# Performance work log

Measured on AMD Instinct MI355X. Metric: run time of the kernel, lower is better.

The kernel has to match this reference:

```python
import jax, jax.numpy as jnp
import numpy as np

B, N, E = 2, 25000, 400000
FC_IN, FC_HID = 64, 256
MUL = 32                     # multiplicity of each output irrep (0e,1e,2e)
W_NUMEL = 3 * MUL            # 96 tensor-product weights per edge
NUM_NEIGHBORS = 16.0


def setup_inputs() -> dict:
    key = jax.random.key(0)
    k1, k2, k3, k4, k5, k6 = jax.random.split(key, 6)
    return {
        "edge_src": jax.random.randint(k1, (E,), 0, N),
        "edge_dst": jax.random.randint(k2, (E,), 0, N),
        "node_emb": jax.random.normal(k3, (B, N, 3), jnp.float32),
        "edge_type": jax.random.normal(k4, (E, FC_IN), jnp.float32),
        "W1": jax.random.normal(k5, (FC_IN, FC_HID), jnp.float32),
        "W2": jax.random.normal(k6, (FC_HID, W_NUMEL), jnp.float32),
    }


def _tensor_product(x, y, w):
    """1o x 1o -> 32x0e + 32x1e + 32x2e, per-edge uvw weights.
    x, y: (B,E,3); w: (E,96). Component-normalized CG coefficients."""
    inv3 = 1.0 / np.sqrt(3.0)
    inv2 = 1.0 / np.sqrt(2.0)
    inv6 = 1.0 / np.sqrt(6.0)
    w0, w1, w2 = w[:, :MUL], w[:, MUL:2 * MUL], w[:, 2 * MUL:]
    # l=0 path: dot product
    s = jnp.sum(x * y, axis=-1) * inv3                     # (B,E)
    out0 = w0[None] * s[..., None]                         # (B,E,32)
    # l=1 path: cross product
    v = jnp.cross(x, y) * inv2                             # (B,E,3)
    out1 = (w1[None, :, :, None] * v[:, :, None, :]).reshape(B, E, 3 * MUL)
    # l=2 path: symmetric traceless combinations
    x0, x1, x2 = x[..., 0], x[..., 1], x[..., 2]
    y0, y1, y2 = y[..., 0], y[..., 1], y[..., 2]
    t = jnp.stack([
        (x0 * y1 + x1 * y0) * inv2,
        (x1 * y2 + x2 * y1) * inv2,
        (x0 * y2 + x2 * y0) * inv2,
        (x0 * y0 - x1 * y1) * inv2,
        (2.0 * x2 * y2 - x0 * y0 - x1 * y1) * inv6,
    ], axis=-1)                                            # (B,E,5)
    out2 = (w2[None, :, :, None] * t[:, :, None, :]).reshape(B, E, 5 * MUL)
    return jnp.concatenate([out0, out1, out2], axis=-1)    # (B,E,288)


def reference(edge_src, edge_dst, node_emb, edge_type, W1, W2):
    # per-edge FC generating TP weights (e3nn FullyConnectedNet-style fan-in norm)
    h = jax.nn.silu(edge_type @ W1 * (1.0 / np.sqrt(FC_IN)))   # (E,256)
    w = (h @ W2) * (1.0 / np.sqrt(FC_HID))                     # (E,96)
    src_emb = node_emb[:, edge_src]                            # (B,E,3)
    dst_emb = node_emb[:, edge_dst]                            # (B,E,3)
    edge_message = _tensor_product(src_emb, dst_emb, w)        # (B,E,288)
    out = jnp.zeros((B, N, edge_message.shape[-1]), edge_message.dtype)
    out = out.at[:, edge_dst].add(edge_message)                # scatter-sum over dst
    return out * (1.0 / np.sqrt(NUM_NEIGHBORS))
```

## Files before the change

### kernel.cpp

```cpp
#include <hip/hip_runtime.h>

#define EDGES 400000
#define NN 25000
#define NCH 288
#define EPA 64
#define NBIN_PAD 25024
#define SWS 68

#define W1FRAG 16384
#define W2FRAG 24576

typedef float f32x4 __attribute__((ext_vector_type(4)));
typedef short short8 __attribute__((ext_vector_type(8)));

__device__ __forceinline__ unsigned short f2bf(float x) {
    unsigned u = __float_as_uint(x);
    unsigned r = (u + 0x7fffu + ((u >> 16) & 1u)) >> 16;
    return (unsigned short)r;
}
__device__ __forceinline__ unsigned short f2bf_t(float x) {
    return (unsigned short)(__float_as_uint(x) >> 16);
}
__device__ __forceinline__ float bf2f(unsigned short h) {
    return __uint_as_float(((unsigned)h) << 16);
}
__device__ __forceinline__ unsigned cvtpk(float a, float b) {
    unsigned r;
    asm("v_cvt_pk_bf16_f32 %0, %1, %2" : "=v"(r) : "v"(a), "v"(b));
    return r;
}
__device__ __forceinline__ float lowf(unsigned u)  { return __uint_as_float(u << 16); }
__device__ __forceinline__ float highf(unsigned u) { return __uint_as_float(u & 0xffff0000u); }

__global__ void k_wfrag(const float* __restrict__ W1, const float* __restrict__ W2,
                        unsigned short* __restrict__ w1h, unsigned short* __restrict__ w1l,
                        unsigned short* __restrict__ w2h, unsigned short* __restrict__ w2l) {
    int i = blockIdx.x * 256 + threadIdx.x;
    if (i < W1FRAG) {
        int j = i & 7, l = (i >> 3) & 63, nt = (i >> 9) & 15, k2 = (i >> 13) & 1;
        int n = nt * 16 + (l & 15), k = k2 * 32 + ((l >> 4) * 8) + j;
        float v = W1[k * 256 + n] * 0.125f;
        unsigned short hb = f2bf(v);
        w1h[i] = hb; w1l[i] = f2bf_t(v - bf2f(hb));
    } else if (i < W1FRAG + W2FRAG) {
        int i2 = i - W1FRAG;
        int j = i2 & 7, l = (i2 >> 3) & 63, r = i2 >> 9;
        int nt = r % 6, k8 = r / 6;
        int n = nt * 16 + (l & 15), k = k8 * 32 + ((l >> 4) * 8) + j;
        float v = W2[k * 96 + n] * 0.015625f;
        unsigned short hb = f2bf(v);
        w2h[i2] = hb; w2l[i2] = f2bf_t(v - bf2f(hb));
    }
}

__global__ void k_hist(const int* __restrict__ edst, unsigned* __restrict__ cnt) {
    int i = blockIdx.x * 256 + threadIdx.x;
    if (i < EDGES) atomicAdd(&cnt[edst[i]], 1u);
}

__global__ __launch_bounds__(1024) void k_scan(const unsigned* __restrict__ cnt,
                                               unsigned* __restrict__ cur) {
    __shared__ unsigned s_wt[16];
    __shared__ unsigned s_carry;
    const int t = threadIdx.x, lane = t & 63, wid = t >> 6;
    if (t == 0) s_carry = 0u;
    __syncthreads();
    for (int base = 0; base < NN; base += 1024) {
        int i = base + t;
        unsigned v = (i < NN) ? cnt[i] : 0u;
        unsigned incl = v;
        #pragma unroll
        for (int d = 1; d < 64; d <<= 1) {
            unsigned u = __shfl_up(incl, d);
            if (lane >= d) incl += u;
        }
        if (lane == 63) s_wt[wid] = incl;
        __syncthreads();
        if (wid == 0 && lane < 16) {
            unsigned wincl = s_wt[lane];
            #pragma unroll
            for (int d = 1; d < 16; d <<= 1) {
                unsigned u = __shfl_up(wincl, d);
                if (lane >= d) wincl += u;
            }
            s_wt[lane] = wincl;
        }
        __syncthreads();
        unsigned waveoff = (wid > 0) ? s_wt[wid - 1] : 0u;
        unsigned carry = s_carry;
        if (i < NN) cur[i] = carry + waveoff + incl - v;
        __syncthreads();
        if (t == 1023) s_carry = carry + s_wt[15];
        __syncthreads();
    }
}

__global__ void k_perm(const int* __restrict__ edst, unsigned* __restrict__ cur,
                       unsigned* __restrict__ perm) {
    int i = blockIdx.x * 256 + threadIdx.x;
    if (i < EDGES) {
        unsigned p = atomicAdd(&cur[edst[i]], 1u);
        perm[p] = (unsigned)i;
    }
}

struct SMemU {
    union {
        struct __align__(16) {
            unsigned short a1h[EPA * 64];
            unsigned short a1l[EPA * 64];
            unsigned short a2h[EPA * 64];
            unsigned short a2l[EPA * 64];
        };
        float sw[96 * SWS];
    };
};

template <bool SORTED>
__global__ __launch_bounds__(256) void conv_fused(
    const int* __restrict__ esrc, const int* __restrict__ edst,
    const float* __restrict__ nemb, const float* __restrict__ etype,
    const unsigned short* __restrict__ w1h, const unsigned short* __restrict__ w1l,
    const unsigned short* __restrict__ w2h, const unsigned short* __restrict__ w2l,
    const unsigned* __restrict__ perm,
    float* __restrict__ out)
{
    __shared__ SMemU U;
    __shared__ __align__(16) float gsm[2][9][SWS];
    __shared__ int s_eidx[EPA], s_dst[EPA];
    __shared__ unsigned s_mlo, s_mhi;

    const int t = threadIdx.x;
    const int lane = t & 63, w = t >> 6;
    const int g = lane >> 4, ln15 = lane & 15;
    const size_t slot0 = (size_t)blockIdx.x * EPA;

    if (t < EPA) {
        int e = SORTED ? (int)perm[slot0 + t] : (int)(slot0 + t);
        s_eidx[t] = e;
        s_dst[t] = edst[e];
    }
    __syncthreads();

    #pragma unroll
    for (int i = 0; i < 4; ++i) {
        int f4 = t + 256 * i;
        int row = f4 >> 4, q = f4 & 15;
        const float4* src = (const float4*)(etype + (size_t)s_eidx[row] * 64);
        float4 v = src[q];
        unsigned hp01 = cvtpk(v.x, v.y), hp23 = cvtpk(v.z, v.w);
        float lo0 = v.x - lowf(hp01), lo1 = v.y - highf(hp01);
        float lo2 = v.z - lowf(hp23), lo3 = v.w - highf(hp23);
        unsigned lp01 = cvtpk(lo0, lo1), lp23 = cvtpk(lo2, lo3);
        int boff = row * 128 + ((q * 8) ^ ((row & 7) << 4));
        *(uint2*)((char*)U.a1h + boff) = make_uint2(hp01, hp23);
        *(uint2*)((char*)U.a1l + boff) = make_uint2(lp01, lp23);
    }
    if (t < EPA * 2) {
        int e = t >> 1, b = t & 1;
        int sn = esrc[s_eidx[e]], dn = s_dst[e];
        const float* xp = nemb + ((size_t)b * NN + sn) * 3;
        const float* yp = nemb + ((size_t)b * NN + dn) * 3;
        float x0 = xp[0], x1 = xp[1], x2 = xp[2];
        float y0 = yp[0], y1 = yp[1], y2 = yp[2];
        const float inv3 = 0.5773502691896258f;
        const float inv2 = 0.7071067811865476f;
        const float inv6 = 0.4082482904638630f;
        gsm[b][0][e] = (x0*y0 + x1*y1 + x2*y2) * inv3;
        gsm[b][1][e] = (x1*y2 - x2*y1) * inv2;
        gsm[b][2][e] = (x2*y0 - x0*y2) * inv2;
        gsm[b][3][e] = (x0*y1 - x1*y0) * inv2;
        gsm[b][4][e] = (x0*y1 + x1*y0) * inv2;
        gsm[b][5][e] = (x1*y2 + x2*y1) * inv2;
        gsm[b][6][e] = (x0*y2 + x2*y0) * inv2;
        gsm[b][7][e] = (x0*y0 - x1*y1) * inv2;
        gsm[b][8][e] = (2.0f*x2*y2 - x0*y0 - x1*y1) * inv6;
    } else if (t < 192) {
        int e = t - 128;
        bool flag = (e > 0) && (s_dst[e] != s_dst[e - 1]);
        unsigned long long bal = __ballot(flag);
        if (e == 0) { s_mlo = (unsigned)bal; s_mhi = (unsigned)(bal >> 32); }
    }
    __syncthreads();

    const int mh = w & 1, nb = 3 * (w >> 1);
    f32x4 acc2[2][3];
    #pragma unroll
    for (int mm = 0; mm < 2; ++mm)
        #pragma unroll
        for (int n = 0; n < 3; ++n)
            #pragma unroll
            for (int r = 0; r < 4; ++r) acc2[mm][n][r] = 0.f;

    #pragma unroll
    for (int qt = 0; qt < 4; ++qt) {
        f32x4 acc1[4];
        #pragma unroll
        for (int m = 0; m < 4; ++m)
            #pragma unroll
            for (int r = 0; r < 4; ++r) acc1[m][r] = 0.f;

        #pragma unroll
        for (int k2 = 0; k2 < 2; ++k2) {
            int idx = ((k2 * 16 + 4 * qt + w) * 64 + lane) * 8;
            short8 wah = *(const short8*)(w1h + idx);
            short8 wal = *(const short8*)(w1l + idx);
            #pragma unroll
            for (int m = 0; m < 4; ++m) {
                int row = m * 16 + ln15;
                int boff = row * 128 + (((k2 * 64) + g * 16) ^ ((row & 7) << 4));
                short8 eth = *(const short8*)((const char*)U.a1h + boff);
                short8 etl = *(const short8*)((const char*)U.a1l + boff);
                acc1[m] = __builtin_amdgcn_mfma_f32_16x16x32_bf16(wah, eth, acc1[m], 0, 0, 0);
                acc1[m] = __builtin_amdgcn_mfma_f32_16x16x32_bf16(wal, eth, acc1[m], 0, 0, 0);
                acc1[m] = __builtin_amdgcn_mfma_f32_16x16x32_bf16(wah, etl, acc1[m], 0, 0, 0);
            }
        }

        #pragma unroll
        for (int m = 0; m < 4; ++m) {
            float p0 = acc1[m][0], p1 = acc1[m][1], p2 = acc1[m][2], p3 = acc1[m][3];
            float s0 = p0 * __builtin_amdgcn_rcpf(1.f + __expf(-p0));
            float s1 = p1 * __builtin_amdgcn_rcpf(1.f + __expf(-p1));
            float s2 = p2 * __builtin_amdgcn_rcpf(1.f + __expf(-p2));
            float s3 = p3 * __builtin_amdgcn_rcpf(1.f + __expf(-p3));
            unsigned hp0 = cvtpk(s0, s1), hp1 = cvtpk(s2, s3);
            float lo0 = s0 - lowf(hp0), lo1 = s1 - highf(hp0);
            float lo2 = s2 - lowf(hp1), lo3 = s3 - highf(hp1);
            unsigned lp0 = cvtpk(lo0, lo1), lp1 = cvtpk(lo2, lo3);
            int e = m * 16 + ln15;
            int boff = e * 128 + ((w * 32 + g * 8) ^ ((ln15 & 7) << 4));
            *(uint2*)((char*)U.a2h + boff) = make_uint2(hp0, hp1);
            *(uint2*)((char*)U.a2l + boff) = make_uint2(lp0, lp1);
        }
        __syncthreads();

        #pragma unroll
        for (int kk = 0; kk < 2; ++kk) {
            int kg = 2 * qt + kk;
            short8 bh[3], bl[3];
            #pragma unroll
            for (int n = 0; n < 3; ++n) {
                int idx = ((kg * 6 + nb + n) * 64 + lane) * 8;
                bh[n] = *(const short8*)(w2h + idx);
                bl[n] = *(const short8*)(w2l + idx);
            }
            #pragma unroll
            for (int mm = 0; mm < 2; ++mm) {
                int row = (2 * mh + mm) * 16 + ln15;
                int boff = row * 128 + ((kk * 64 + g * 16) ^ ((ln15 & 7) << 4));
                short8 ah = *(const short8*)((const char*)U.a2h + boff);
                short8 al = *(const short8*)((const char*)U.a2l + boff);
                #pragma unroll
                for (int n = 0; n < 3; ++n) {
                    acc2[mm][n] = __builtin_amdgcn_mfma_f32_16x16x32_bf16(ah, bh[n], acc2[mm][n], 0, 0, 0);
                    acc2[mm][n] = __builtin_amdgcn_mfma_f32_16x16x32_bf16(ah, bl[n], acc2[mm][n], 0, 0, 0);
                    acc2[mm][n] = __builtin_amdgcn_mfma_f32_16x16x32_bf16(al, bh[n], acc2[mm][n], 0, 0, 0);
                }
            }
        }
        __syncthreads();
    }

    #pragma unroll
    for (int mm = 0; mm < 2; ++mm) {
        #pragma unroll
        for (int n = 0; n < 3; ++n) {
            int c = (nb + n) * 16 + ln15;
            int e_base = (2 * mh + mm) * 16 + g * 4;
            *(f32x4*)&U.sw[c * SWS + e_base] = acc2[mm][n];
        }
    }
    __syncthreads();

    {
        unsigned mlo = __builtin_amdgcn_readfirstlane(s_mlo);
        unsigned mhi = __builtin_amdgcn_readfirstlane(s_mhi);
        for (int idx = t; idx < NCH * 2; idx += 256) {
            int b = idx >= NCH;
            int c = idx - b * NCH;
            unsigned wi, gi;
            if (c < 32)       { wi = c;                          gi = 0; }
            else if (c < 128) { unsigned q = c - 32;  wi = 32 + q / 3u; gi = 1 + q % 3u; }
            else              { unsigned q = c - 128; wi = 64 + q / 5u; gi = 4 + q % 5u; }
            float* base = out + (size_t)b * NN * NCH + c;
            float acc = 0.f;
            int rs = 0;
            #pragma unroll
            for (int q4 = 0; q4 < 16; ++q4) {
                f32x4 wv = *(const f32x4*)&U.sw[wi * SWS + q4 * 4];
                f32x4 gv = *(const f32x4*)&gsm[b][gi][q4 * 4];
                #pragma unroll
                for (int j = 0; j < 4; ++j) {
                    int e = q4 * 4 + j;
                    bool bnd = (e < 32) ? ((mlo >> e) & 1u) : ((mhi >> (e - 32)) & 1u);
                    if (e && bnd) {
                        float* addr = base + (size_t)s_dst[e - 1] * NCH;
                        if (SORTED && rs > 0) *addr = acc;
                        else atomicAdd(addr, acc);
                        acc = 0.f; rs = e;
                    }
                    acc = fmaf(wv[j], gv[j], acc);
                }
            }
            atomicAdd(base + (size_t)s_dst[EPA - 1] * NCH, acc);
        }
    }
}

extern "C" void kernel_launch(void* const* d_in, const int* in_sizes, int n_in,
                              void* d_out, int out_size, void* d_ws, size_t ws_size,
                              hipStream_t stream) {
    const int*   esrc  = (const int*)d_in[0];
    const int*   edst  = (const int*)d_in[1];
    const float* nemb  = (const float*)d_in[2];
    const float* etype = (const float*)d_in[3];
    const float* W1    = (const float*)d_in[4];
    const float* W2    = (const float*)d_in[5];
    float* out = (float*)d_out;

    hipMemsetAsync(out, 0, (size_t)out_size * sizeof(float), stream);

    const size_t frag_bytes = (size_t)(2 * W1FRAG + 2 * W2FRAG) * sizeof(unsigned short);
    unsigned short* w1h = (unsigned short*)d_ws;
    unsigned short* w1l = w1h + W1FRAG;
    unsigned short* w2h = w1l + W1FRAG;
    unsigned short* w2l = w2h + W2FRAG;

    size_t o_cnt  = frag_bytes;
    size_t o_cur  = o_cnt + (size_t)NBIN_PAD * 4;
    size_t o_perm = o_cur + (size_t)NBIN_PAD * 4;
    size_t need_sort = o_perm + (size_t)EDGES * 4;

    k_wfrag<<<(W1FRAG + W2FRAG + 255) / 256, 256, 0, stream>>>(W1, W2, w1h, w1l, w2h, w2l);

    if (ws_size >= need_sort) {
        unsigned* cnt  = (unsigned*)((char*)d_ws + o_cnt);
        unsigned* cur  = (unsigned*)((char*)d_ws + o_cur);
        unsigned* perm = (unsigned*)((char*)d_ws + o_perm);
        hipMemsetAsync(cnt, 0, (size_t)NBIN_PAD * 4, stream);
        k_hist<<<(EDGES + 255) / 256, 256, 0, stream>>>(edst, cnt);
        k_scan<<<1, 1024, 0, stream>>>(cnt, cur);
        k_perm<<<(EDGES + 255) / 256, 256, 0, stream>>>(edst, cur, perm);
        conv_fused<true><<<EDGES / EPA, 256, 0, stream>>>(
            esrc, edst, nemb, etype, w1h, w1l, w2h, w2l, perm, out);
    } else {
        conv_fused<false><<<EDGES / EPA, 256, 0, stream>>>(
            esrc, edst, nemb, etype, w1h, w1l, w2h, w2l, nullptr, out);
    }
}
```

Before: 216.6 us.

## Double edges per block to 128 with 512 threads and parallelize the prefix scan

The fused conv kernel now handles 128 edges per block with 8 waves, so each block scatters fewer partial sums at run boundaries and segment accumulations in sorted order span longer runs. This should reduce atomic traffic and per-block overhead. The single-block serial scan is replaced by a three-kernel block-parallel scan, trading one long single-block launch for two extra short launches. Larger shared memory per block may reduce occupancy.

New measurement: 298.0 us. +37.6%, slower.

```diff
diff --git a/kernel.cpp b/kernel.cpp
--- a/kernel.cpp
+++ b/kernel.cpp
@@ -3,9 +3,9 @@
 #define EDGES 400000
 #define NN 25000
 #define NCH 288
-#define EPA 64
+#define EPA 128
 #define NBIN_PAD 25024
-#define SWS 68
+#define SWS 132
 
 #define W1FRAG 16384
 #define W2FRAG 24576
@@ -58,41 +58,52 @@
     if (i < EDGES) atomicAdd(&cnt[edst[i]], 1u);
 }
 
-__global__ __launch_bounds__(1024) void k_scan(const unsigned* __restrict__ cnt,
-                                               unsigned* __restrict__ cur) {
+__global__ __launch_bounds__(1024) void k_scanA(const unsigned* __restrict__ cnt,
+                                                unsigned* __restrict__ cur,
+                                                unsigned* __restrict__ tot) {
     __shared__ unsigned s_wt[16];
-    __shared__ unsigned s_carry;
     const int t = threadIdx.x, lane = t & 63, wid = t >> 6;
-    if (t == 0) s_carry = 0u;
-    __syncthreads();
-    for (int base = 0; base < NN; base += 1024) {
-        int i = base + t;
-        unsigned v = (i < NN) ? cnt[i] : 0u;
-        unsigned incl = v;
-        #pragma unroll
-        for (int d = 1; d < 64; d <<= 1) {
-            unsigned u = __shfl_up(incl, d);
-            if (lane >= d) incl += u;
-        }
-        if (lane == 63) s_wt[wid] = incl;
-        __syncthreads();
-        if (wid == 0 && lane < 16) {
-            unsigned wincl = s_wt[lane];
-            #pragma unroll
-            for (int d = 1; d < 16; d <<= 1) {
-                unsigned u = __shfl_up(wincl, d);
-                if (lane >= d) wincl += u;
-            }
-            s_wt[lane] = wincl;
-        }
-        __syncthreads();
-        unsigned waveoff = (wid > 0) ? s_wt[wid - 1] : 0u;
-        unsigned carry = s_carry;
-        if (i < NN) cur[i] = carry + waveoff + incl - v;
-        __syncthreads();
-        if (t == 1023) s_carry = carry + s_wt[15];
-        __syncthreads();
-    }
+    int i = blockIdx.x * 1024 + t;
+    unsigned v = (i < NN) ? cnt[i] : 0u;
+    unsigned incl = v;
+    #pragma unroll
+    for (int d = 1; d < 64; d <<= 1) {
+        unsigned u = __shfl_up(incl, d);
+        if (lane >= d) incl += u;
+    }
+    if (lane == 63) s_wt[wid] = incl;
+    __syncthreads();
+    if (wid == 0 && lane < 16) {
+        unsigned wincl = s_wt[lane];
+        #pragma unroll
+        for (int d = 1; d < 16; d <<= 1) {
+            unsigned u = __shfl_up(wincl, d);
+            if (lane >= d) wincl += u;
+        }
+        s_wt[lane] = wincl;
+    }
+    __syncthreads();
+    unsigned waveoff = (wid > 0) ? s_wt[wid - 1] : 0u;
+    if (i < NN) cur[i] = waveoff + incl - v;
+    if (t == 0) tot[blockIdx.x] = s_wt[15];
+}
+
+__global__ void k_scanB(unsigned* __restrict__ tot, unsigned* __restrict__ toff, int nblk) {
+    int lane = threadIdx.x;
+    unsigned v = (lane < nblk) ? tot[lane] : 0u;
+    unsigned incl = v;
+    #pragma unroll
+    for (int d = 1; d < 64; d <<= 1) {
+        unsigned u = __shfl_up(incl, d);
+        if (lane >= d) incl += u;
+    }
+    if (lane < nblk) toff[lane] = incl - v;
+}
+
+__global__ __launch_bounds__(1024) void k_scanC(unsigned* __restrict__ cur,
+                                                const unsigned* __restrict__ toff) {
+    int i = blockIdx.x * 1024 + threadIdx.x;
+    if (i < NN) cur[i] += toff[blockIdx.x];
 }
 
 __global__ void k_perm(const int* __restrict__ edst, unsigned* __restrict__ cur,
@@ -117,7 +128,7 @@
 };
 
 template <bool SORTED>
-__global__ __launch_bounds__(256) void conv_fused(
+__global__ __launch_bounds__(512) void conv_fused(
     const int* __restrict__ esrc, const int* __restrict__ edst,
     const float* __restrict__ nemb, const float* __restrict__ etype,
     const unsigned short* __restrict__ w1h, const unsigned short* __restrict__ w1l,
@@ -128,7 +139,7 @@
     __shared__ SMemU U;
     __shared__ __align__(16) float gsm[2][9][SWS];
     __shared__ int s_eidx[EPA], s_dst[EPA];
-    __shared__ unsigned s_mlo, s_mhi;
+    __shared__ unsigned s_m[4];
 
     const int t = threadIdx.x;
     const int lane = t & 63, w = t >> 6;
@@ -144,7 +155,7 @@
 
     #pragma unroll
     for (int i = 0; i < 4; ++i) {
-        int f4 = t + 256 * i;
+        int f4 = t + 512 * i;
         int row = f4 >> 4, q = f4 & 15;
         const float4* src = (const float4*)(etype + (size_t)s_eidx[row] * 64);
         float4 v = src[q];
@@ -175,15 +186,22 @@
         gsm[b][6][e] = (x0*y2 + x2*y0) * inv2;
         gsm[b][7][e] = (x0*y0 - x1*y1) * inv2;
         gsm[b][8][e] = (2.0f*x2*y2 - x0*y0 - x1*y1) * inv6;
-    } else if (t < 192) {
-        int e = t - 128;
-        bool flag = (e > 0) && (s_dst[e] != s_dst[e - 1]);
+    } else if (t < EPA * 3) {
+        int l = t - EPA * 2;
+        bool flag = (l > 0) && (s_dst[l] != s_dst[l - 1]);
         unsigned long long bal = __ballot(flag);
-        if (e == 0) { s_mlo = (unsigned)bal; s_mhi = (unsigned)(bal >> 32); }
-    }
-    __syncthreads();
-
-    const int mh = w & 1, nb = 3 * (w >> 1);
+        if ((l & 63) == 0) {
+            int half = l >> 6;
+            s_m[half * 2 + 0] = (unsigned)bal;
+            s_m[half * 2 + 1] = (unsigned)(bal >> 32);
+        }
+    }
+    __syncthreads();
+
+    const int eh = w >> 2;
+    const int n4 = w & 3;
+    const int eq = w >> 1;
+    const int nb = 3 * (w & 1);
     f32x4 acc2[2][3];
     #pragma unroll
     for (int mm = 0; mm < 2; ++mm)
@@ -202,12 +220,12 @@
 
         #pragma unroll
         for (int k2 = 0; k2 < 2; ++k2) {
-            int idx = ((k2 * 16 + 4 * qt + w) * 64 + lane) * 8;
+            int idx = ((k2 * 16 + 4 * qt + n4) * 64 + lane) * 8;
             short8 wah = *(const short8*)(w1h + idx);
             short8 wal = *(const short8*)(w1l + idx);
             #pragma unroll
             for (int m = 0; m < 4; ++m) {
-                int row = m * 16 + ln15;
+                int row = (4 * eh + m) * 16 + ln15;
                 int boff = row * 128 + (((k2 * 64) + g * 16) ^ ((row & 7) << 4));
                 short8 eth = *(const short8*)((const char*)U.a1h + boff);
                 short8 etl = *(const short8*)((const char*)U.a1l + boff);
@@ -228,8 +246,8 @@
             float lo0 = s0 - lowf(hp0), lo1 = s1 - highf(hp0);
             float lo2 = s2 - lowf(hp1), lo3 = s3 - highf(hp1);
             unsigned lp0 = cvtpk(lo0, lo1), lp1 = cvtpk(lo2, lo3);
-            int e = m * 16 + ln15;
-            int boff = e * 128 + ((w * 32 + g * 8) ^ ((ln15 & 7) << 4));
+            int e = (4 * eh + m) * 16 + ln15;
+            int boff = e * 128 + ((n4 * 32 + g * 8) ^ ((ln15 & 7) << 4));
             *(uint2*)((char*)U.a2h + boff) = make_uint2(hp0, hp1);
             *(uint2*)((char*)U.a2l + boff) = make_uint2(lp0, lp1);
         }
@@ -247,7 +265,7 @@
             }
             #pragma unroll
             for (int mm = 0; mm < 2; ++mm) {
-                int row = (2 * mh + mm) * 16 + ln15;
+                int row = (2 * eq + mm) * 16 + ln15;
                 int boff = row * 128 + ((kk * 64 + g * 16) ^ ((ln15 & 7) << 4));
                 short8 ah = *(const short8*)((const char*)U.a2h + boff);
                 short8 al = *(const short8*)((const char*)U.a2l + boff);
@@ -267,16 +285,18 @@
         #pragma unroll
         for (int n = 0; n < 3; ++n) {
             int c = (nb + n) * 16 + ln15;
-            int e_base = (2 * mh + mm) * 16 + g * 4;
+            int e_base = (2 * eq + mm) * 16 + g * 4;
             *(f32x4*)&U.sw[c * SWS + e_base] = acc2[mm][n];
         }
     }
     __syncthreads();
 
     {
-        unsigned mlo = __builtin_amdgcn_readfirstlane(s_mlo);
-        unsigned mhi = __builtin_amdgcn_readfirstlane(s_mhi);
-        for (int idx = t; idx < NCH * 2; idx += 256) {
+        unsigned mk0 = __builtin_amdgcn_readfirstlane(s_m[0]);
+        unsigned mk1 = __builtin_amdgcn_readfirstlane(s_m[1]);
+        unsigned mk2 = __builtin_amdgcn_readfirstlane(s_m[2]);
+        unsigned mk3 = __builtin_amdgcn_readfirstlane(s_m[3]);
+        for (int idx = t; idx < NCH * 2; idx += 512) {
             int b = idx >= NCH;
             int c = idx - b * NCH;
             unsigned wi, gi;
@@ -287,13 +307,14 @@
             float acc = 0.f;
             int rs = 0;
             #pragma unroll
-            for (int q4 = 0; q4 < 16; ++q4) {
+            for (int q4 = 0; q4 < EPA / 4; ++q4) {
                 f32x4 wv = *(const f32x4*)&U.sw[wi * SWS + q4 * 4];
                 f32x4 gv = *(const f32x4*)&gsm[b][gi][q4 * 4];
                 #pragma unroll
                 for (int j = 0; j < 4; ++j) {
                     int e = q4 * 4 + j;
-                    bool bnd = (e < 32) ? ((mlo >> e) & 1u) : ((mhi >> (e - 32)) & 1u);
+                    unsigned word = (e < 32) ? mk0 : (e < 64) ? mk1 : (e < 96) ? mk2 : mk3;
+                    bool bnd = (word >> (e & 31)) & 1u;
                     if (e && bnd) {
                         float* addr = base + (size_t)s_dst[e - 1] * NCH;
                         if (SORTED && rs > 0) *addr = acc;
@@ -327,9 +348,12 @@
     unsigned short* w2h = w1l + W1FRAG;
     unsigned short* w2l = w2h + W2FRAG;
 
+    const int NSCAN = (NN + 1023) / 1024;
     size_t o_cnt  = frag_bytes;
     size_t o_cur  = o_cnt + (size_t)NBIN_PAD * 4;
-    size_t o_perm = o_cur + (size_t)NBIN_PAD * 4;
+    size_t o_tot  = o_cur + (size_t)NBIN_PAD * 4;
+    size_t o_toff = o_tot + 128;
+    size_t o_perm = o_toff + 128;
     size_t need_sort = o_perm + (size_t)EDGES * 4;
 
     k_wfrag<<<(W1FRAG + W2FRAG + 255) / 256, 256, 0, stream>>>(W1, W2, w1h, w1l, w2h, w2l);
@@ -337,15 +361,19 @@
     if (ws_size >= need_sort) {
         unsigned* cnt  = (unsigned*)((char*)d_ws + o_cnt);
         unsigned* cur  = (unsigned*)((char*)d_ws + o_cur);
+        unsigned* tot  = (unsigned*)((char*)d_ws + o_tot);
+        unsigned* toff = (unsigned*)((char*)d_ws + o_toff);
         unsigned* perm = (unsigned*)((char*)d_ws + o_perm);
         hipMemsetAsync(cnt, 0, (size_t)NBIN_PAD * 4, stream);
         k_hist<<<(EDGES + 255) / 256, 256, 0, stream>>>(edst, cnt);
-        k_scan<<<1, 1024, 0, stream>>>(cnt, cur);
+        k_scanA<<<NSCAN, 1024, 0, stream>>>(cnt, cur, tot);
+        k_scanB<<<1, 64, 0, stream>>>(tot, toff, NSCAN);
+        k_scanC<<<NSCAN, 1024, 0, stream>>>(cur, toff);
         k_perm<<<(EDGES + 255) / 256, 256, 0, stream>>>(edst, cur, perm);
-        conv_fused<true><<<EDGES / EPA, 256, 0, stream>>>(
+        conv_fused<true><<<EDGES / EPA, 512, 0, stream>>>(
             esrc, edst, nemb, etype, w1h, w1l, w2h, w2l, perm, out);
     } else {
-        conv_fused<false><<<EDGES / EPA, 256, 0, stream>>>(
+        conv_fused<false><<<EDGES / EPA, 512, 0, stream>>>(
             esrc, edst, nemb, etype, w1h, w1l, w2h, w2l, nullptr, out);
     }
 }
```

## Parallelize prefix scan across blocks and add fast path for boundary-free edge groups

Applied to the files above, without the earlier changes.

Replaces the single-block serial-loop exclusive scan over node counts with a three-kernel multi-block scan: per-block scan, a scan of block totals, then an offset add. The scatter loop in the fused conv kernel now tests a 4-bit nibble of the segment-boundary mask and runs four plain FMAs when no boundary falls in that group, skipping per-edge branch checks. This targets the latency of the 25-iteration single-block scan and the branch overhead in the output accumulation loop, at the cost of two extra kernel launches.

Result: faster. 197.4 us, median of 2 (-8.8%).

```diff
diff --git a/kernel.cpp b/kernel.cpp
--- a/kernel.cpp
+++ b/kernel.cpp
@@ -58,41 +58,52 @@
     if (i < EDGES) atomicAdd(&cnt[edst[i]], 1u);
 }
 
-__global__ __launch_bounds__(1024) void k_scan(const unsigned* __restrict__ cnt,
-                                               unsigned* __restrict__ cur) {
+__global__ __launch_bounds__(1024) void k_scanA(const unsigned* __restrict__ cnt,
+                                                unsigned* __restrict__ cur,
+                                                unsigned* __restrict__ tot) {
     __shared__ unsigned s_wt[16];
-    __shared__ unsigned s_carry;
     const int t = threadIdx.x, lane = t & 63, wid = t >> 6;
-    if (t == 0) s_carry = 0u;
-    __syncthreads();
-    for (int base = 0; base < NN; base += 1024) {
-        int i = base + t;
-        unsigned v = (i < NN) ? cnt[i] : 0u;
-        unsigned incl = v;
-        #pragma unroll
-        for (int d = 1; d < 64; d <<= 1) {
-            unsigned u = __shfl_up(incl, d);
-            if (lane >= d) incl += u;
-        }
-        if (lane == 63) s_wt[wid] = incl;
-        __syncthreads();
-        if (wid == 0 && lane < 16) {
-            unsigned wincl = s_wt[lane];
-            #pragma unroll
-            for (int d = 1; d < 16; d <<= 1) {
-                unsigned u = __shfl_up(wincl, d);
-                if (lane >= d) wincl += u;
-            }
-            s_wt[lane] = wincl;
-        }
-        __syncthreads();
-        unsigned waveoff = (wid > 0) ? s_wt[wid - 1] : 0u;
-        unsigned carry = s_carry;
-        if (i < NN) cur[i] = carry + waveoff + incl - v;
-        __syncthreads();
-        if (t == 1023) s_carry = carry + s_wt[15];
-        __syncthreads();
-    }
+    int i = blockIdx.x * 1024 + t;
+    unsigned v = (i < NN) ? cnt[i] : 0u;
+    unsigned incl = v;
+    #pragma unroll
+    for (int d = 1; d < 64; d <<= 1) {
+        unsigned u = __shfl_up(incl, d);
+        if (lane >= d) incl += u;
+    }
+    if (lane == 63) s_wt[wid] = incl;
+    __syncthreads();
+    if (wid == 0 && lane < 16) {
+        unsigned wincl = s_wt[lane];
+        #pragma unroll
+        for (int d = 1; d < 16; d <<= 1) {
+            unsigned u = __shfl_up(wincl, d);
+            if (lane >= d) wincl += u;
+        }
+        s_wt[lane] = wincl;
+    }
+    __syncthreads();
+    unsigned waveoff = (wid > 0) ? s_wt[wid - 1] : 0u;
+    if (i < NN) cur[i] = waveoff + incl - v;
+    if (t == 0) tot[blockIdx.x] = s_wt[15];
+}
+
+__global__ void k_scanB(unsigned* __restrict__ tot, unsigned* __restrict__ toff, int nblk) {
+    int lane = threadIdx.x;
+    unsigned v = (lane < nblk) ? tot[lane] : 0u;
+    unsigned incl = v;
+    #pragma unroll
+    for (int d = 1; d < 64; d <<= 1) {
+        unsigned u = __shfl_up(incl, d);
+        if (lane >= d) incl += u;
+    }
+    if (lane < nblk) toff[lane] = incl - v;
+}
+
+__global__ __launch_bounds__(1024) void k_scanC(unsigned* __restrict__ cur,
+                                                const unsigned* __restrict__ toff) {
+    int i = blockIdx.x * 1024 + threadIdx.x;
+    if (i < NN) cur[i] += toff[blockIdx.x];
 }
 
 __global__ void k_perm(const int* __restrict__ edst, unsigned* __restrict__ cur,
@@ -290,17 +301,25 @@
             for (int q4 = 0; q4 < 16; ++q4) {
                 f32x4 wv = *(const f32x4*)&U.sw[wi * SWS + q4 * 4];
                 f32x4 gv = *(const f32x4*)&gsm[b][gi][q4 * 4];
-                #pragma unroll
-                for (int j = 0; j < 4; ++j) {
-                    int e = q4 * 4 + j;
-                    bool bnd = (e < 32) ? ((mlo >> e) & 1u) : ((mhi >> (e - 32)) & 1u);
-                    if (e && bnd) {
-                        float* addr = base + (size_t)s_dst[e - 1] * NCH;
-                        if (SORTED && rs > 0) *addr = acc;
-                        else atomicAdd(addr, acc);
-                        acc = 0.f; rs = e;
+                unsigned word = (q4 < 8) ? mlo : mhi;
+                unsigned nib = (word >> ((q4 * 4) & 31)) & 0xFu;
+                if (nib == 0u) {
+                    acc = fmaf(wv[0], gv[0], acc);
+                    acc = fmaf(wv[1], gv[1], acc);
+                    acc = fmaf(wv[2], gv[2], acc);
+                    acc = fmaf(wv[3], gv[3], acc);
+                } else {
+                    #pragma unroll
+                    for (int j = 0; j < 4; ++j) {
+                        int e = q4 * 4 + j;
+                        if (e && ((nib >> j) & 1u)) {
+                            float* addr = base + (size_t)s_dst[e - 1] * NCH;
+                            if (SORTED && rs > 0) *addr = acc;
+                            else atomicAdd(addr, acc);
+                            acc = 0.f; rs = e;
+                        }
+                        acc = fmaf(wv[j], gv[j], acc);
                     }
-                    acc = fmaf(wv[j], gv[j], acc);
                 }
             }
             atomicAdd(base + (size_t)s_dst[EPA - 1] * NCH, acc);
@@ -327,9 +346,12 @@
     unsigned short* w2h = w1l + W1FRAG;
     unsigned short* w2l = w2h + W2FRAG;
 
+    const int NSCAN = (NN + 1023) / 1024;
     size_t o_cnt  = frag_bytes;
     size_t o_cur  = o_cnt + (size_t)NBIN_PAD * 4;
-    size_t o_perm = o_cur + (size_t)NBIN_PAD * 4;
+    size_t o_tot  = o_cur + (size_t)NBIN_PAD * 4;
+    size_t o_toff = o_tot + 128;
+    size_t o_perm = o_toff + 128;
     size_t need_sort = o_perm + (size_t)EDGES * 4;
 
     k_wfrag<<<(W1FRAG + W2FRAG + 255) / 256, 256, 0, stream>>>(W1, W2, w1h, w1l, w2h, w2l);
@@ -337,10 +359,14 @@
     if (ws_size >= need_sort) {
         unsigned* cnt  = (unsigned*)((char*)d_ws + o_cnt);
         unsigned* cur  = (unsigned*)((char*)d_ws + o_cur);
+        unsigned* tot  = (unsigned*)((char*)d_ws + o_tot);
+        unsigned* toff = (unsigned*)((char*)d_ws + o_toff);
         unsigned* perm = (unsigned*)((char*)d_ws + o_perm);
         hipMemsetAsync(cnt, 0, (size_t)NBIN_PAD * 4, stream);
         k_hist<<<(EDGES + 255) / 256, 256, 0, stream>>>(edst, cnt);
-        k_scan<<<1, 1024, 0, stream>>>(cnt, cur);
+        k_scanA<<<NSCAN, 1024, 0, stream>>>(cnt, cur, tot);
+        k_scanB<<<1, 64, 0, stream>>>(tot, toff, NSCAN);
+        k_scanC<<<NSCAN, 1024, 0, stream>>>(cur, toff);
         k_perm<<<(EDGES + 255) / 256, 256, 0, stream>>>(edst, cur, perm);
         conv_fused<true><<<EDGES / EPA, 256, 0, stream>>>(
             esrc, edst, nemb, etype, w1h, w1l, w2h, w2l, perm, out);
```
